# Performance work log

Measured on AMD Instinct MI355X. Metric: run time of the kernel, lower is better.

## Reference

```python
import jax, jax.numpy as jnp
import numpy as np

B, T, N, F_IN = 32, 64, 128, 16
H, SOUT = 64, 16
D = N * SOUT            # transformer d_model = 2048
NHEADS, DH = 16, 128
DFF, LAYERS = 2048, 2
NCLASSES, OUT = 8, 10
THR = 0.004             # edge threshold on sigmoid(V)/N


def setup_inputs():
    key = jax.random.key(0)
    ks = iter(jax.random.split(key, 40))
    r = lambda *s: jax.random.normal(next(ks), s, jnp.float32) * 0.02
    return {
        'X': jax.random.normal(next(ks), (B, T, N * F_IN), jnp.float32),
        'V_Adap': jax.random.normal(next(ks), (NCLASSES, N, N), jnp.float32),
        'Wl': r(F_IN, H), 'bl': jnp.zeros((H,)),
        'Wr': r(F_IN, H), 'br': jnp.zeros((H,)),
        'att': jax.random.normal(next(ks), (H,), jnp.float32) * 0.1,
        'gat_bias': jnp.zeros((H,)),
        'Wfc': r(H, SOUT), 'bfc': jnp.zeros((SOUT,)),
        'Wq': r(LAYERS, D, D), 'bq': jnp.zeros((LAYERS, D)),
        'Wk': r(LAYERS, D, D), 'bk': jnp.zeros((LAYERS, D)),
        'Wv': r(LAYERS, D, D), 'bv': jnp.zeros((LAYERS, D)),
        'Wo': r(LAYERS, D, D), 'bo': jnp.zeros((LAYERS, D)),
        'ln1_g': jnp.ones((LAYERS, D)), 'ln1_b': jnp.zeros((LAYERS, D)),
        'W1': r(LAYERS, D, DFF), 'b1': jnp.zeros((LAYERS, DFF)),
        'W2': r(LAYERS, DFF, D), 'b2': jnp.zeros((LAYERS, D)),
        'ln2_g': jnp.ones((LAYERS, D)), 'ln2_b': jnp.zeros((LAYERS, D)),
        'Wout': r(D, OUT), 'bout': jnp.zeros((OUT,)),
        'class_idx': 2,
    }


def _ln(x, g, b):
    mu = jnp.mean(x, -1, keepdims=True)
    var = jnp.var(x, -1, keepdims=True)
    return (x - mu) / jnp.sqrt(var + 1e-5) * g + b


def reference(X, V_Adap, Wl, bl, Wr, br, att, gat_bias, Wfc, bfc,
              Wq, bq, Wk, bk, Wv, bv, Wo, bo, ln1_g, ln1_b,
              W1, b1, W2, b2, ln2_g, ln2_b, Wout, bout, class_idx):
    # dynamic adjacency: sigmoid + scale + threshold (data-dependent sparsity as a mask)
    A = jax.nn.sigmoid(V_Adap[class_idx]) / N
    mask = (A > THR) | jnp.eye(N, dtype=bool)   # GATv2Conv default add_self_loops

    def gat_step(x_t):                           # x_t: (B, N, F_IN)
        xl = x_t @ Wl + bl                       # source transform (B, N, H)
        xr = x_t @ Wr + br                       # target transform (B, N, H)
        s = jax.nn.leaky_relu(xl[:, :, None, :] + xr[:, None, :, :], 0.2)  # (B, src, dst, H)
        e = jnp.where(mask[None], jnp.einsum('bijh,h->bij', s, att), -1e9)
        alpha = jax.nn.softmax(e, axis=1)        # softmax over sources per target node
        out = jnp.einsum('bij,bih->bjh', alpha, xl) + gat_bias
        return out @ Wfc + bfc                   # (B, N, SOUT)

    Xr = X.reshape(B, T, N, F_IN).transpose(1, 0, 2, 3)   # (T, B, N, F)
    spatial = jax.lax.map(gat_step, Xr)                   # (T, B, N, SOUT)
    h = spatial.transpose(1, 0, 2, 3).reshape(B, T, D)

    # post-norm TransformerEncoder (torch defaults: relu, d_ff=2048, no dropout at eval)
    for l in range(LAYERS):
        q = (h @ Wq[l] + bq[l]).reshape(B, T, NHEADS, DH).transpose(0, 2, 1, 3)
        k = (h @ Wk[l] + bk[l]).reshape(B, T, NHEADS, DH).transpose(0, 2, 1, 3)
        v = (h @ Wv[l] + bv[l]).reshape(B, T, NHEADS, DH).transpose(0, 2, 1, 3)
        aw = jax.nn.softmax(jnp.einsum('bhqd,bhkd->bhqk', q, k) / np.float32(np.sqrt(DH)), axis=-1)
        ao = jnp.einsum('bhqk,bhkd->bhqd', aw, v).transpose(0, 2, 1, 3).reshape(B, T, D)
        h = _ln(h + ao @ Wo[l] + bo[l], ln1_g[l], ln1_b[l])
        ff = jax.nn.relu(h @ W1[l] + b1[l]) @ W2[l] + b2[l]
        h = _ln(h + ff, ln2_g[l], ln2_b[l])

    return h[:, -1, :] @ Wout + bout             # (B, OUT)
```

## Files before the change

kernel.cpp:

```cpp
#include <hip/hip_runtime.h>
#include <cstdint>
#include <cstddef>


typedef unsigned short u16;
typedef __bf16 bf16x8 __attribute__((ext_vector_type(8)));
typedef float f32x4 __attribute__((ext_vector_type(4)));
typedef unsigned int u32x4 __attribute__((ext_vector_type(4)));
typedef float f32x4v __attribute__((ext_vector_type(4)));
typedef unsigned short u16x4 __attribute__((ext_vector_type(4)));

__device__ __forceinline__ u16 f2b(float f) {
  union { float f; unsigned u; } x; x.f = f;
  unsigned r = x.u + 0x7fffu + ((x.u >> 16) & 1u);
  return (u16)(r >> 16);
}
__device__ __forceinline__ float b2f(u16 s) {
  union { unsigned u; float f; } x; x.u = ((unsigned)s) << 16;
  return x.f;
}
__device__ __forceinline__ float b2f_lo(unsigned q) {
  union { unsigned u; float f; } x; x.u = q << 16;
  return x.f;
}
__device__ __forceinline__ float b2f_hi(unsigned q) {
  union { unsigned u; float f; } x; x.u = q & 0xffff0000u;
  return x.f;
}

__device__ __forceinline__ void gload_lds16(const void* g, void* l) {
  __builtin_amdgcn_global_load_lds(
      (const __attribute__((address_space(1))) unsigned int*)g,
      (__attribute__((address_space(3))) unsigned int*)l, 16, 0, 0);
}

__global__ __launch_bounds__(1024) void gat_kernel(
    const float* __restrict__ X, const float* __restrict__ V_Adap,
    const int* __restrict__ class_idx,
    const float* __restrict__ Wl, const float* __restrict__ bl,
    const float* __restrict__ Wr, const float* __restrict__ br,
    const float* __restrict__ att, const float* __restrict__ gat_bias,
    const float* __restrict__ Wfc, const float* __restrict__ bfc,
    float* __restrict__ h_f32, u16* __restrict__ h_b16)
{
  const int bt = blockIdx.x;
  const int tid = threadIdx.x;

  __shared__ __align__(16) float xlT[64 * 132];
  __shared__ __align__(16) float xrT[64 * 132];
  __shared__ __align__(16) u16   xlTb[64 * 136];
  __shared__ __align__(16) u16   esbT[128 * 136];
  __shared__ __align__(16) u16   aggb[128 * 72];
  __shared__ __align__(16) float WlT[64 * 20];
  __shared__ __align__(16) float WrT[64 * 20];
  __shared__ __align__(16) float WfcT[16 * 66];
  __shared__ float atts[64], bls[64], brs[64], gbias[64], bfcs[16];
  __shared__ float cls[128], crs[128], inv_s[128];
  __shared__ float red[8 * 128];

  {
    const int h = tid >> 4, f = tid & 15;
    WlT[h * 20 + f] = Wl[f * 64 + h];
    WrT[h * 20 + f] = Wr[f * 64 + h];
    WfcT[f * 66 + h] = Wfc[h * 16 + f];
  }
  if (tid < 64) { atts[tid] = att[tid]; bls[tid] = bl[tid]; brs[tid] = br[tid]; gbias[tid] = gat_bias[tid]; }
  if (tid < 16) bfcs[tid] = bfc[tid];
  const int cidx = *class_idx;
  __syncthreads();

  {
    const int n = tid >> 3, hq = tid & 7;
    const float* xp = X + (size_t)bt * 2048 + n * 16;
    float xv[16];
    #pragma unroll
    for (int f4 = 0; f4 < 4; f4++) {
      f32x4v t4 = ((const f32x4v*)xp)[f4];
      xv[f4 * 4 + 0] = t4[0]; xv[f4 * 4 + 1] = t4[1];
      xv[f4 * 4 + 2] = t4[2]; xv[f4 * 4 + 3] = t4[3];
    }
    #pragma unroll
    for (int k = 0; k < 8; k++) {
      const int h = hq + 8 * k;
      float al = bls[h], ar = brs[h];
      #pragma unroll
      for (int f4 = 0; f4 < 4; f4++) {
        f32x4v wl = *(const f32x4v*)&WlT[h * 20 + f4 * 4];
        f32x4v wr = *(const f32x4v*)&WrT[h * 20 + f4 * 4];
        #pragma unroll
        for (int f = 0; f < 4; f++) {
          al = fmaf(xv[f4 * 4 + f], wl[f], al);
          ar = fmaf(xv[f4 * 4 + f], wr[f], ar);
        }
      }
      xlT[h * 132 + n] = al;
      xrT[h * 132 + n] = ar;
      xlTb[h * 136 + n] = f2b(al);
    }
  }
  __syncthreads();

  if (tid < 256) {
    const int n = tid & 127;
    const float* srcT = (tid < 128) ? xlT : xrT;
    float s = 0.f;
    for (int h = 0; h < 64; h++) s = fmaf(atts[h], srcT[h * 132 + n], s);
    if (tid < 128) cls[n] = s; else crs[n] = s;
  }
  __syncthreads();

  {
    const int i0 = (tid >> 5) * 4;
    const int j0 = (tid & 31) * 4;
    float acc[4][4] = {};
    #pragma unroll 2
    for (int h = 0; h < 64; h++) {
      const float ah = atts[h];
      f32x4v xa = *(const f32x4v*)&xlT[h * 132 + i0];
      f32x4v xb = *(const f32x4v*)&xrT[h * 132 + j0];
      #pragma unroll
      for (int a = 0; a < 4; a++)
        #pragma unroll
        for (int b = 0; b < 4; b++)
          acc[a][b] = fmaf(ah, __builtin_fabsf(xa[a] + xb[b]), acc[a][b]);
    }
    const float* Vc = V_Adap + (size_t)cidx * 16384;
    float vm[4][4];
    #pragma unroll
    for (int a = 0; a < 4; a++) {
      f32x4v vc = *(const f32x4v*)&Vc[(size_t)(i0 + a) * 128 + j0];
      #pragma unroll
      for (int b = 0; b < 4; b++) vm[a][b] = vc[b];
    }
    #pragma unroll
    for (int b = 0; b < 4; b++) {
      const int j = j0 + b;
      const float ej = 0.6f * crs[j];
      u16x4 pk;
      #pragma unroll
      for (int a = 0; a < 4; a++) {
        const int i = i0 + a;
        const float e = ej + 0.6f * cls[i] + 0.4f * acc[a][b];
        const bool m = (vm[a][b] > 0.04800922f) || (i == j);
        pk[a] = f2b(m ? e : -1e9f);
      }
      *(u16x4*)&esbT[j * 136 + i0] = pk;
    }
  }
  __syncthreads();

  {
    const int j = tid >> 3, c = tid & 7;
    u16* rp = &esbT[j * 136 + c * 16];
    float ps = 0.f;
    #pragma unroll
    for (int half = 0; half < 2; half++) {
      u32x4 q = *(u32x4*)(rp + half * 8);
      #pragma unroll
      for (int w2 = 0; w2 < 4; w2++) {
        const float p0 = __expf(b2f_lo(q[w2]));
        const float p1 = __expf(b2f_hi(q[w2]));
        ps += p0 + p1;
        q[w2] = (unsigned)f2b(p0) | ((unsigned)f2b(p1) << 16);
      }
      *(u32x4*)(rp + half * 8) = q;
    }
    red[c * 128 + j] = ps;
  }
  __syncthreads();
  if (tid < 128) {
    float s = 0.f;
    #pragma unroll
    for (int c = 0; c < 8; c++) s += red[c * 128 + tid];
    inv_s[tid] = 1.f / s;
  }
  __syncthreads();

  {
    const int w = tid >> 6, lane = tid & 63;
    const int lq = lane >> 4, lr = lane & 15;
    const int jt = w >> 1, ht0 = (w & 1) * 2;
    f32x4 acc2[2] = {};
    #pragma unroll
    for (int ks = 0; ks < 4; ks++) {
      const bf16x8 af = __builtin_bit_cast(bf16x8,
          *(const u32x4*)&esbT[(jt * 16 + lr) * 136 + ks * 32 + lq * 8]);
      #pragma unroll
      for (int t = 0; t < 2; t++) {
        const bf16x8 bfb = __builtin_bit_cast(bf16x8,
            *(const u32x4*)&xlTb[((ht0 + t) * 16 + lr) * 136 + ks * 32 + lq * 8]);
        acc2[t] = __builtin_amdgcn_mfma_f32_16x16x32_bf16(af, bfb, acc2[t], 0, 0, 0);
      }
    }
    #pragma unroll
    for (int t = 0; t < 2; t++) {
      const int h = (ht0 + t) * 16 + lr;
      const float gb = gbias[h];
      #pragma unroll
      for (int r = 0; r < 4; r++) {
        const int j = jt * 16 + lq * 4 + r;
        aggb[j * 72 + h] = f2b(acc2[t][r] * inv_s[j] + gb);
      }
    }
  }
  __syncthreads();

  {
    const int j = tid >> 3, s0 = (tid & 7) * 2;
    float o0 = bfcs[s0], o1 = bfcs[s0 + 1];
    #pragma unroll
    for (int h8 = 0; h8 < 8; h8++) {
      u32x4 q = *(const u32x4*)&aggb[j * 72 + h8 * 8];
      #pragma unroll
      for (int w2 = 0; w2 < 4; w2++) {
        const int h = h8 * 8 + w2 * 2;
        const float a0 = b2f_lo(q[w2]);
        const float a1 = b2f_hi(q[w2]);
        o0 = fmaf(a0, WfcT[s0 * 66 + h], o0);
        o1 = fmaf(a0, WfcT[(s0 + 1) * 66 + h], o1);
        o0 = fmaf(a1, WfcT[s0 * 66 + h + 1], o0);
        o1 = fmaf(a1, WfcT[(s0 + 1) * 66 + h + 1], o1);
      }
    }
    const size_t off = (size_t)bt * 2048 + j * 16 + s0;
    h_f32[off] = o0; h_f32[off + 1] = o1;
    h_b16[off] = f2b(o0); h_b16[off + 1] = f2b(o1);
  }
}

struct TransArgs {
  const float* s0; const float* s1; const float* s2;
  u16* d0; u16* d1; u16* d2;
};

__global__ __launch_bounds__(256) void transpose_cast(TransArgs p)
{
  const float* src = (blockIdx.z == 0) ? p.s0 : (blockIdx.z == 1) ? p.s1 : p.s2;
  u16* dst = (blockIdx.z == 0) ? p.d0 : (blockIdx.z == 1) ? p.d1 : p.d2;
  __shared__ u16 tile[64][66];
  const int k0 = blockIdx.y * 64, n0 = blockIdx.x * 64;
  const int tid = threadIdx.x;
  const int c = tid & 63, rb = tid >> 6;
  #pragma unroll
  for (int r = 0; r < 16; r++) {
    const int k = rb + r * 4;
    tile[k][c] = f2b(src[(size_t)(k0 + k) * 2048 + n0 + c]);
  }
  __syncthreads();
  #pragma unroll
  for (int r = 0; r < 16; r++) {
    const int n = rb + r * 4;
    dst[(size_t)(n0 + n) * 2048 + k0 + c] = tile[c][n];
  }
}

struct GemmArgs {
  const u16* A;
  const u16* Bt0; const u16* Bt1; const u16* Bt2;
  const float* b0; const float* b1; const float* b2;
  void* C0; void* C1; void* C2;
  int N; int K;
};

template <int MODE>
__global__ __launch_bounds__(256) void gemm_bt(GemmArgs g)
{
  const int z = blockIdx.z;
  const u16* Bt = (z == 0) ? g.Bt0 : (z == 1) ? g.Bt1 : g.Bt2;
  const float* bias = (z == 0) ? g.b0 : (z == 1) ? g.b1 : g.b2;
  void* C = (z == 0) ? g.C0 : (z == 1) ? g.C1 : g.C2;
  const int N = g.N, K = g.K;
  const int m0 = blockIdx.y * 128, n0 = blockIdx.x * 128;

  __shared__ __align__(16) u16 As[2][128 * 32];
  __shared__ __align__(16) u16 Bs[2][128 * 32];

  const int tid = threadIdx.x;
  const int lane = tid & 63, w = tid >> 6;
  const int srow = w * 16 + (lane >> 2);
  const int scol = ((lane & 3) ^ ((lane >> 2) & 3)) * 8;
  const u16* gA = g.A + (size_t)(m0 + srow) * K + scol;
  const u16* gB = Bt + (size_t)(n0 + srow) * K + scol;
  const int lbase = (w * 16) * 32;

  const int wm = (w >> 1) * 64, wn = (w & 1) * 64;
  const int lq = lane >> 4, lr = lane & 15;
  const int csw = (lr & 3) << 3;

  f32x4 acc[4][4] = {};
  const int NT = K >> 5;

  auto stage = [&](int buf, int kt) {
    const int kk = kt << 5;
    #pragma unroll
    for (int c = 0; c < 2; c++) {
      gload_lds16(gA + (size_t)(c * 64) * K + kk, &As[buf][lbase + c * 64 * 32]);
      gload_lds16(gB + (size_t)(c * 64) * K + kk, &Bs[buf][lbase + c * 64 * 32]);
    }
  };
  auto compute = [&](int buf) {
    bf16x8 af[4], bfr[4];
    #pragma unroll
    for (int i = 0; i < 4; i++) {
      af[i] = __builtin_bit_cast(bf16x8,
          *(const u32x4*)&As[buf][(wm + i * 16 + lr) * 32 + ((lq * 8) ^ csw)]);
      bfr[i] = __builtin_bit_cast(bf16x8,
          *(const u32x4*)&Bs[buf][(wn + i * 16 + lr) * 32 + ((lq * 8) ^ csw)]);
    }
    #pragma unroll
    for (int mi = 0; mi < 4; mi++)
      #pragma unroll
      for (int ni = 0; ni < 4; ni++)
        acc[mi][ni] = __builtin_amdgcn_mfma_f32_16x16x32_bf16(af[mi], bfr[ni], acc[mi][ni], 0, 0, 0);
  };

  stage(0, 0);
  __syncthreads();
  int cur = 0;
  for (int kt = 0; kt + 1 < NT; ++kt) {
    stage(cur ^ 1, kt + 1);
    compute(cur);
    __syncthreads();
    cur ^= 1;
  }
  compute(cur);

  #pragma unroll
  for (int ni = 0; ni < 4; ni++) {
    const int col = n0 + wn + ni * 16 + lr;
    const float bv = bias[col];
    #pragma unroll
    for (int mi = 0; mi < 4; mi++) {
      #pragma unroll
      for (int r = 0; r < 4; r++) {
        const int row = m0 + wm + mi * 16 + lq * 4 + r;
        float v = acc[mi][ni][r] + bv;
        if (MODE == 0) {
          ((float*)C)[(size_t)row * N + col] = v;
        } else {
          if (MODE == 2) v = fmaxf(v, 0.f);
          ((u16*)C)[(size_t)row * N + col] = f2b(v);
        }
      }
    }
  }
}

template <int MODE>
__global__ __launch_bounds__(256) void gemm_bt64(GemmArgs g)
{
  const u16* Bt = g.Bt0;
  const float* bias = g.b0;
  void* C = g.C0;
  const int N = g.N, K = g.K;
  const int m0 = blockIdx.y * 128, n0 = blockIdx.x * 64;

  __shared__ __align__(16) u16 As[2][128 * 64];
  __shared__ __align__(16) u16 Bs[2][64 * 64];

  const int tid = threadIdx.x;
  const int lane = tid & 63, w = tid >> 6;
  const int srow = w * 8 + (lane >> 3);
  const int scol = ((lane & 7) ^ (lane >> 3)) * 8;
  const u16* gA = g.A + (size_t)(m0 + srow) * K + scol;
  const u16* gB = Bt + (size_t)(n0 + srow) * K + scol;
  const int lbase = (w * 8) * 64;

  const int wm = w * 32;
  const int lq = lane >> 4, lr = lane & 15;
  const int csw = (lr & 7) << 3;

  f32x4 acc[2][4] = {};
  const int NT = K >> 6;

  auto stage = [&](int buf, int kt) {
    const int kk = kt << 6;
    #pragma unroll
    for (int c = 0; c < 4; c++)
      gload_lds16(gA + (size_t)(c * 32) * K + kk, &As[buf][lbase + c * 32 * 64]);
    #pragma unroll
    for (int c = 0; c < 2; c++)
      gload_lds16(gB + (size_t)(c * 32) * K + kk, &Bs[buf][lbase + c * 32 * 64]);
  };
  auto compute = [&](int buf) {
    #pragma unroll
    for (int ks = 0; ks < 2; ks++) {
      bf16x8 af[2], bfr[4];
      #pragma unroll
      for (int i = 0; i < 2; i++)
        af[i] = __builtin_bit_cast(bf16x8,
            *(const u32x4*)&As[buf][(wm + i * 16 + lr) * 64 + ((ks * 32 + lq * 8) ^ csw)]);
      #pragma unroll
      for (int i = 0; i < 4; i++)
        bfr[i] = __builtin_bit_cast(bf16x8,
            *(const u32x4*)&Bs[buf][(i * 16 + lr) * 64 + ((ks * 32 + lq * 8) ^ csw)]);
      #pragma unroll
      for (int mi = 0; mi < 2; mi++)
        #pragma unroll
        for (int ni = 0; ni < 4; ni++)
          acc[mi][ni] = __builtin_amdgcn_mfma_f32_16x16x32_bf16(af[mi], bfr[ni], acc[mi][ni], 0, 0, 0);
    }
  };

  stage(0, 0);
  __syncthreads();
  int cur = 0;
  for (int kt = 0; kt + 1 < NT; ++kt) {
    stage(cur ^ 1, kt + 1);
    compute(cur);
    __syncthreads();
    cur ^= 1;
  }
  compute(cur);

  #pragma unroll
  for (int ni = 0; ni < 4; ni++) {
    const int col = n0 + ni * 16 + lr;
    const float bv = bias[col];
    #pragma unroll
    for (int mi = 0; mi < 2; mi++) {
      #pragma unroll
      for (int r = 0; r < 4; r++) {
        const int row = m0 + wm + mi * 16 + lq * 4 + r;
        float v = acc[mi][ni][r] + bv;
        if (MODE == 0) {
          ((float*)C)[(size_t)row * N + col] = v;
        } else {
          if (MODE == 2) v = fmaxf(v, 0.f);
          ((u16*)C)[(size_t)row * N + col] = f2b(v);
        }
      }
    }
  }
}

__global__ __launch_bounds__(256) void attn_kernel(
    const u16* __restrict__ Qb, const u16* __restrict__ Kb,
    const u16* __restrict__ Vb, u16* __restrict__ AOb)
{
  const int head = blockIdx.x, b = blockIdx.y;
  const int tid = threadIdx.x;
  __shared__ __align__(16) float qs[64 * 132];
  __shared__ __align__(16) float ks[64 * 132];
  __shared__ __align__(16) float vs[64 * 128];
  __shared__ __align__(16) float ss[64 * 65];
  const size_t base = ((size_t)b * 64) * 2048 + (size_t)head * 128;

  for (int idx = tid; idx < 1024; idx += 256) {
    const int t_ = idx >> 4, d8 = (idx & 15) * 8;
    const size_t gp = base + (size_t)t_ * 2048 + d8;
    const u32x4 q = *(const u32x4*)(Qb + gp);
    const u32x4 k = *(const u32x4*)(Kb + gp);
    const u32x4 v = *(const u32x4*)(Vb + gp);
    f32x4 q0 = {b2f_lo(q[0]), b2f_hi(q[0]), b2f_lo(q[1]), b2f_hi(q[1])};
    f32x4 q1 = {b2f_lo(q[2]), b2f_hi(q[2]), b2f_lo(q[3]), b2f_hi(q[3])};
    f32x4 k0 = {b2f_lo(k[0]), b2f_hi(k[0]), b2f_lo(k[1]), b2f_hi(k[1])};
    f32x4 k1 = {b2f_lo(k[2]), b2f_hi(k[2]), b2f_lo(k[3]), b2f_hi(k[3])};
    f32x4 v0 = {b2f_lo(v[0]), b2f_hi(v[0]), b2f_lo(v[1]), b2f_hi(v[1])};
    f32x4 v1 = {b2f_lo(v[2]), b2f_hi(v[2]), b2f_lo(v[3]), b2f_hi(v[3])};
    *(f32x4*)&qs[t_ * 132 + d8] = q0; *(f32x4*)&qs[t_ * 132 + d8 + 4] = q1;
    *(f32x4*)&ks[t_ * 132 + d8] = k0; *(f32x4*)&ks[t_ * 132 + d8 + 4] = k1;
    *(f32x4*)&vs[t_ * 128 + d8] = v0; *(f32x4*)&vs[t_ * 128 + d8 + 4] = v1;
  }
  __syncthreads();

  {
    const int i0 = (tid >> 4) * 4, j0 = tid & 15;
    float acc[4][4] = {};
    #pragma unroll 2
    for (int d0 = 0; d0 < 128; d0 += 4) {
      f32x4 qv[4], kv[4];
      #pragma unroll
      for (int a = 0; a < 4; a++) qv[a] = *(const f32x4*)&qs[(i0 + a) * 132 + d0];
      #pragma unroll
      for (int c = 0; c < 4; c++) kv[c] = *(const f32x4*)&ks[(j0 + c * 16) * 132 + d0];
      #pragma unroll
      for (int a = 0; a < 4; a++)
        #pragma unroll
        for (int c = 0; c < 4; c++)
          #pragma unroll
          for (int e = 0; e < 4; e++)
            acc[a][c] = fmaf(qv[a][e], kv[c][e], acc[a][c]);
    }
    const float sc = 0.08838834764831845f;
    #pragma unroll
    for (int a = 0; a < 4; a++)
      #pragma unroll
      for (int c = 0; c < 4; c++)
        ss[(i0 + a) * 65 + j0 + c * 16] = acc[a][c] * sc;
  }
  __syncthreads();

  {
    const int row = tid >> 2;
    float* rp = &ss[row * 65 + (tid & 3) * 16];
    float mx = -3e38f;
    #pragma unroll
    for (int j = 0; j < 16; j++) mx = fmaxf(mx, rp[j]);
    mx = fmaxf(mx, __shfl_xor(mx, 1, 64));
    mx = fmaxf(mx, __shfl_xor(mx, 2, 64));
    float s = 0.f;
    #pragma unroll
    for (int j = 0; j < 16; j++) { const float p = __expf(rp[j] - mx); rp[j] = p; s += p; }
    s += __shfl_xor(s, 1, 64);
    s += __shfl_xor(s, 2, 64);
    const float inv = 1.f / s;
    #pragma unroll
    for (int j = 0; j < 16; j++) rp[j] *= inv;
  }
  __syncthreads();

  {
    const int i0 = (tid >> 4) * 4, d0 = (tid & 15) * 8;
    float o[4][8] = {};
    for (int j = 0; j < 64; j++) {
      float pv[4];
      #pragma unroll
      for (int a = 0; a < 4; a++) pv[a] = ss[(i0 + a) * 65 + j];
      f32x4v v0 = *(const f32x4v*)&vs[j * 128 + d0];
      f32x4v v1 = *(const f32x4v*)&vs[j * 128 + d0 + 4];
      float vv[8] = {v0[0], v0[1], v0[2], v0[3], v1[0], v1[1], v1[2], v1[3]};
      #pragma unroll
      for (int a = 0; a < 4; a++)
        #pragma unroll
        for (int c = 0; c < 8; c++)
          o[a][c] = fmaf(pv[a], vv[c], o[a][c]);
    }
    #pragma unroll
    for (int a = 0; a < 4; a++)
      #pragma unroll
      for (int c = 0; c < 8; c++)
        AOb[base + (size_t)(i0 + a) * 2048 + d0 + c] = f2b(o[a][c]);
  }
}

__global__ __launch_bounds__(256) void ln_kernel(
    const float* __restrict__ hin, const float* __restrict__ delta,
    const float* __restrict__ gamma, const float* __restrict__ beta,
    float* __restrict__ hout, u16* __restrict__ bout_)
{
  const int token = blockIdx.x, tid = threadIdx.x;
  const size_t off = (size_t)token * 2048;
  __shared__ float red[8];
  f32x4 v[2];
  float s = 0.f;
  #pragma unroll
  for (int r = 0; r < 2; r++) {
    const int i = r * 1024 + tid * 4;
    const f32x4 a = *(const f32x4*)(hin + off + i);
    const f32x4 b = *(const f32x4*)(delta + off + i);
    v[r] = a + b;
    s += v[r][0] + v[r][1] + v[r][2] + v[r][3];
  }
  #pragma unroll
  for (int o = 32; o > 0; o >>= 1) s += __shfl_down(s, o, 64);
  if ((tid & 63) == 0) red[tid >> 6] = s;
  __syncthreads();
  const float mean = (red[0] + red[1] + red[2] + red[3]) * (1.f / 2048.f);
  float s2 = 0.f;
  #pragma unroll
  for (int r = 0; r < 2; r++)
    #pragma unroll
    for (int e = 0; e < 4; e++) { const float d = v[r][e] - mean; s2 = fmaf(d, d, s2); }
  #pragma unroll
  for (int o = 32; o > 0; o >>= 1) s2 += __shfl_down(s2, o, 64);
  if ((tid & 63) == 0) red[4 + (tid >> 6)] = s2;
  __syncthreads();
  const float var = (red[4] + red[5] + red[6] + red[7]) * (1.f / 2048.f);
  const float rstd = rsqrtf(var + 1e-5f);
  #pragma unroll
  for (int r = 0; r < 2; r++) {
    const int i = r * 1024 + tid * 4;
    const f32x4 gm = *(const f32x4*)(gamma + i);
    const f32x4 bt = *(const f32x4*)(beta + i);
    f32x4 y;
    u16x4 pb;
    #pragma unroll
    for (int e = 0; e < 4; e++) {
      y[e] = (v[r][e] - mean) * rstd * gm[e] + bt[e];
      pb[e] = f2b(y[e]);
    }
    *(f32x4*)(hout + off + i) = y;
    *(u16x4*)(bout_ + off + i) = pb;
  }
}

__global__ __launch_bounds__(256) void final_kernel(
    const float* __restrict__ h, const float* __restrict__ Wout,
    const float* __restrict__ bout, float* __restrict__ out)
{
  const int b = blockIdx.x, tid = threadIdx.x;
  __shared__ float row[2048];
  __shared__ float part[256];
  const float* hr = h + ((size_t)b * 64 + 63) * 2048;
  for (int i = tid; i < 2048; i += 256) row[i] = hr[i];
  __syncthreads();
  const int o = tid & 15, ch = tid >> 4;
  float s = 0.f;
  if (o < 10) {
    const int i0 = ch * 128;
    for (int i = i0; i < i0 + 128; i++) s = fmaf(row[i], Wout[(size_t)i * 10 + o], s);
  }
  part[tid] = s;
  __syncthreads();
  if (tid < 10) {
    float t = bout[tid];
    for (int c2 = 0; c2 < 16; c2++) t += part[c2 * 16 + tid];
    out[(size_t)b * 10 + tid] = t;
  }
}

extern "C" void kernel_launch(void* const* d_in, const int* in_sizes, int n_in,
                              void* d_out, int out_size, void* d_ws, size_t ws_size,
                              hipStream_t stream)
{
  const float* X        = (const float*)d_in[0];
  const float* V_Adap   = (const float*)d_in[1];
  const float* Wl       = (const float*)d_in[2];
  const float* bl       = (const float*)d_in[3];
  const float* Wr       = (const float*)d_in[4];
  const float* br       = (const float*)d_in[5];
  const float* att      = (const float*)d_in[6];
  const float* gat_bias = (const float*)d_in[7];
  const float* Wfc      = (const float*)d_in[8];
  const float* bfc      = (const float*)d_in[9];
  const float* Wq       = (const float*)d_in[10];
  const float* bq       = (const float*)d_in[11];
  const float* Wk       = (const float*)d_in[12];
  const float* bk       = (const float*)d_in[13];
  const float* Wv       = (const float*)d_in[14];
  const float* bv       = (const float*)d_in[15];
  const float* Wo       = (const float*)d_in[16];
  const float* bo       = (const float*)d_in[17];
  const float* ln1_g    = (const float*)d_in[18];
  const float* ln1_b    = (const float*)d_in[19];
  const float* W1       = (const float*)d_in[20];
  const float* b1       = (const float*)d_in[21];
  const float* W2       = (const float*)d_in[22];
  const float* b2       = (const float*)d_in[23];
  const float* ln2_g    = (const float*)d_in[24];
  const float* ln2_b    = (const float*)d_in[25];
  const float* WoutP    = (const float*)d_in[26];
  const float* boutP    = (const float*)d_in[27];
  const int*   class_idx = (const int*)d_in[28];

  char* ws = (char*)d_ws;
  const size_t MB = (size_t)1 << 20;
  float* h_f32 = (float*)(ws);
  u16*   h_b16 = (u16*)(ws + 16 * MB);
  u16*   Qb    = (u16*)(ws + 24 * MB);
  u16*   Kb    = (u16*)(ws + 32 * MB);
  u16*   Vb    = (u16*)(ws + 40 * MB);
  u16*   AOb   = (u16*)(ws + 48 * MB);
  float* tmp   = (float*)(ws + 56 * MB);
  u16*   ff1b  = (u16*)(ws + 72 * MB);
  u16*   Wt0   = (u16*)(ws + 80 * MB);
  u16*   Wt1   = (u16*)(ws + 88 * MB);
  u16*   Wt2   = (u16*)(ws + 96 * MB);

  gat_kernel<<<2048, 1024, 0, stream>>>(X, V_Adap, class_idx, Wl, bl, Wr, br,
                                        att, gat_bias, Wfc, bfc, h_f32, h_b16);

  const size_t DD = 2048ull * 2048ull;
  for (int l = 0; l < 2; l++) {
    const size_t wofs = (size_t)l * DD;
    const size_t bofs = (size_t)l * 2048;

    transpose_cast<<<dim3(32, 32, 3), 256, 0, stream>>>(
        TransArgs{Wq + wofs, Wk + wofs, Wv + wofs, Wt0, Wt1, Wt2});
    gemm_bt<1><<<dim3(16, 16, 3), 256, 0, stream>>>(
        GemmArgs{h_b16, Wt0, Wt1, Wt2, bq + bofs, bk + bofs, bv + bofs,
                 Qb, Kb, Vb, 2048, 2048});

    attn_kernel<<<dim3(16, 32), 256, 0, stream>>>(Qb, Kb, Vb, AOb);

    transpose_cast<<<dim3(32, 32, 3), 256, 0, stream>>>(
        TransArgs{Wo + wofs, W1 + wofs, W2 + wofs, Wt0, Wt1, Wt2});

    gemm_bt64<0><<<dim3(32, 16), 256, 0, stream>>>(
        GemmArgs{AOb, Wt0, nullptr, nullptr, bo + bofs, nullptr, nullptr,
                 tmp, nullptr, nullptr, 2048, 2048});
    ln_kernel<<<2048, 256, 0, stream>>>(h_f32, tmp, ln1_g + bofs, ln1_b + bofs,
                                        h_f32, h_b16);

    gemm_bt64<2><<<dim3(32, 16), 256, 0, stream>>>(
        GemmArgs{h_b16, Wt1, nullptr, nullptr, b1 + bofs, nullptr, nullptr,
                 ff1b, nullptr, nullptr, 2048, 2048});

    gemm_bt64<0><<<dim3(32, 16), 256, 0, stream>>>(
        GemmArgs{ff1b, Wt2, nullptr, nullptr, b2 + bofs, nullptr, nullptr,
                 tmp, nullptr, nullptr, 2048, 2048});
    ln_kernel<<<2048, 256, 0, stream>>>(h_f32, tmp, ln2_g + bofs, ln2_b + bofs,
                                        h_f32, h_b16);
  }

  final_kernel<<<32, 256, 0, stream>>>(h_f32, WoutP, boutP, (float*)d_out);
}
```

Baseline: 907.0 us.

## Restructure GAT projection, attention-coefficient reduction and edge-score tiling

```diff
diff --git a/kernel.cpp b/kernel.cpp
--- a/kernel.cpp
+++ b/kernel.cpp
@@ -6,6 +6,7 @@
 typedef unsigned short u16;
 typedef __bf16 bf16x8 __attribute__((ext_vector_type(8)));
 typedef float f32x4 __attribute__((ext_vector_type(4)));
+typedef float f32x2 __attribute__((ext_vector_type(2)));
 typedef unsigned int u32x4 __attribute__((ext_vector_type(4)));
 typedef float f32x4v __attribute__((ext_vector_type(4)));
 typedef unsigned short u16x4 __attribute__((ext_vector_type(4)));
@@ -58,6 +59,8 @@
   __shared__ float cls[128], crs[128], inv_s[128];
   __shared__ float red[8 * 128];
 
+  float* scratchX = (float*)aggb;
+
   {
     const int h = tid >> 4, f = tid & 15;
     WlT[h * 20 + f] = Wl[f * 64 + h];
@@ -66,85 +69,110 @@
   }
   if (tid < 64) { atts[tid] = att[tid]; bls[tid] = bl[tid]; brs[tid] = br[tid]; gbias[tid] = gat_bias[tid]; }
   if (tid < 16) bfcs[tid] = bfc[tid];
+  if (tid < 512)
+    ((f32x4*)scratchX)[tid] = ((const f32x4*)(X + (size_t)bt * 2048))[tid];
   const int cidx = *class_idx;
   __syncthreads();
 
   {
-    const int n = tid >> 3, hq = tid & 7;
-    const float* xp = X + (size_t)bt * 2048 + n * 16;
-    float xv[16];
+    const int h = tid & 63, ng = tid >> 6;
+    f32x4 wl4[4], wr4[4];
     #pragma unroll
     for (int f4 = 0; f4 < 4; f4++) {
-      f32x4v t4 = ((const f32x4v*)xp)[f4];
-      xv[f4 * 4 + 0] = t4[0]; xv[f4 * 4 + 1] = t4[1];
-      xv[f4 * 4 + 2] = t4[2]; xv[f4 * 4 + 3] = t4[3];
-    }
-    #pragma unroll
-    for (int k = 0; k < 8; k++) {
-      const int h = hq + 8 * k;
-      float al = bls[h], ar = brs[h];
+      wl4[f4] = *(const f32x4*)&WlT[h * 20 + f4 * 4];
+      wr4[f4] = *(const f32x4*)&WrT[h * 20 + f4 * 4];
+    }
+    const float blh = bls[h], brh = brs[h];
+    float al8[8], ar8[8];
+    #pragma unroll
+    for (int t = 0; t < 8; t++) {
+      const int n = ng * 8 + t;
+      float al = blh, ar = brh;
       #pragma unroll
       for (int f4 = 0; f4 < 4; f4++) {
-        f32x4v wl = *(const f32x4v*)&WlT[h * 20 + f4 * 4];
-        f32x4v wr = *(const f32x4v*)&WrT[h * 20 + f4 * 4];
+        const f32x4 xv = *(const f32x4*)&scratchX[n * 16 + f4 * 4];
         #pragma unroll
         for (int f = 0; f < 4; f++) {
-          al = fmaf(xv[f4 * 4 + f], wl[f], al);
-          ar = fmaf(xv[f4 * 4 + f], wr[f], ar);
+          al = fmaf(xv[f], wl4[f4][f], al);
+          ar = fmaf(xv[f], wr4[f4][f], ar);
         }
       }
-      xlT[h * 132 + n] = al;
-      xrT[h * 132 + n] = ar;
-      xlTb[h * 136 + n] = f2b(al);
-    }
-  }
-  __syncthreads();
-
+      al8[t] = al; ar8[t] = ar;
+    }
+    *(f32x4*)&xlT[h * 132 + ng * 8]     = *(f32x4*)&al8[0];
+    *(f32x4*)&xlT[h * 132 + ng * 8 + 4] = *(f32x4*)&al8[4];
+    *(f32x4*)&xrT[h * 132 + ng * 8]     = *(f32x4*)&ar8[0];
+    *(f32x4*)&xrT[h * 132 + ng * 8 + 4] = *(f32x4*)&ar8[4];
+    u16 pb[8];
+    #pragma unroll
+    for (int t = 0; t < 8; t++) pb[t] = f2b(al8[t]);
+    *(u16x4*)&xlTb[h * 136 + ng * 8]     = *(u16x4*)&pb[0];
+    *(u16x4*)&xlTb[h * 136 + ng * 8 + 4] = *(u16x4*)&pb[4];
+  }
+  __syncthreads();
+
+  {
+    const int n = tid & 127, g = tid >> 7;
+    const float* srcT = (g < 4) ? xlT : xrT;
+    const int h0 = (g & 3) * 16;
+    float s = 0.f;
+    #pragma unroll
+    for (int hh = 0; hh < 16; hh++)
+      s = fmaf(atts[h0 + hh], srcT[(h0 + hh) * 132 + n], s);
+    red[g * 128 + n] = s;
+  }
+  __syncthreads();
   if (tid < 256) {
     const int n = tid & 127;
-    const float* srcT = (tid < 128) ? xlT : xrT;
-    float s = 0.f;
-    for (int h = 0; h < 64; h++) s = fmaf(atts[h], srcT[h * 132 + n], s);
+    const int base = (tid < 128) ? 0 : 4;
+    const float s = ((red[base * 128 + n] + red[(base + 1) * 128 + n])
+                   + red[(base + 2) * 128 + n]) + red[(base + 3) * 128 + n];
     if (tid < 128) cls[n] = s; else crs[n] = s;
   }
   __syncthreads();
 
   {
-    const int i0 = (tid >> 5) * 4;
-    const int j0 = (tid & 31) * 4;
-    float acc[4][4] = {};
-    #pragma unroll 2
+    const int i0 = (tid >> 6) * 8;
+    const int j0 = (tid & 63) * 2;
+    float acc[8][2] = {};
+    #pragma unroll 8
     for (int h = 0; h < 64; h++) {
-      const float ah = atts[h];
-      f32x4v xa = *(const f32x4v*)&xlT[h * 132 + i0];
-      f32x4v xb = *(const f32x4v*)&xrT[h * 132 + j0];
-      #pragma unroll
-      for (int a = 0; a < 4; a++)
-        #pragma unroll
-        for (int b = 0; b < 4; b++)
-          acc[a][b] = fmaf(ah, __builtin_fabsf(xa[a] + xb[b]), acc[a][b]);
+      const float ah = att[h];
+      const f32x4 xa0 = *(const f32x4*)&xlT[h * 132 + i0];
+      const f32x4 xa1 = *(const f32x4*)&xlT[h * 132 + i0 + 4];
+      const f32x2 xb  = *(const f32x2*)&xrT[h * 132 + j0];
+      #pragma unroll
+      for (int a = 0; a < 4; a++) {
+        acc[a][0]     = fmaf(ah, __builtin_fabsf(xa0[a] + xb[0]), acc[a][0]);
+        acc[a][1]     = fmaf(ah, __builtin_fabsf(xa0[a] + xb[1]), acc[a][1]);
+        acc[4 + a][0] = fmaf(ah, __builtin_fabsf(xa1[a] + xb[0]), acc[4 + a][0]);
+        acc[4 + a][1] = fmaf(ah, __builtin_fabsf(xa1[a] + xb[1]), acc[4 + a][1]);
+      }
     }
     const float* Vc = V_Adap + (size_t)cidx * 16384;
-    float vm[4][4];
-    #pragma unroll
-    for (int a = 0; a < 4; a++) {
-      f32x4v vc = *(const f32x4v*)&Vc[(size_t)(i0 + a) * 128 + j0];
-      #pragma unroll
-      for (int b = 0; b < 4; b++) vm[a][b] = vc[b];
-    }
-    #pragma unroll
-    for (int b = 0; b < 4; b++) {
+    float vm[8][2];
+    #pragma unroll
+    for (int a = 0; a < 8; a++) {
+      const f32x2 vc = *(const f32x2*)&Vc[(size_t)(i0 + a) * 128 + j0];
+      vm[a][0] = vc[0]; vm[a][1] = vc[1];
+    }
+    const f32x4 cl0 = *(const f32x4*)&cls[i0];
+    const f32x4 cl1 = *(const f32x4*)&cls[i0 + 4];
+    float cli[8] = {cl0[0], cl0[1], cl0[2], cl0[3], cl1[0], cl1[1], cl1[2], cl1[3]};
+    #pragma unroll
+    for (int b = 0; b < 2; b++) {
       const int j = j0 + b;
       const float ej = 0.6f * crs[j];
-      u16x4 pk;
-      #pragma unroll
-      for (int a = 0; a < 4; a++) {
+      u16 pk[8];
+      #pragma unroll
+      for (int a = 0; a < 8; a++) {
         const int i = i0 + a;
-        const float e = ej + 0.6f * cls[i] + 0.4f * acc[a][b];
+        const float e = ej + 0.6f * cli[a] + 0.4f * acc[a][b];
         const bool m = (vm[a][b] > 0.04800922f) || (i == j);
         pk[a] = f2b(m ? e : -1e9f);
       }
-      *(u16x4*)&esbT[j * 136 + i0] = pk;
+      *(u16x4*)&esbT[j * 136 + i0]     = *(u16x4*)&pk[0];
+      *(u16x4*)&esbT[j * 136 + i0 + 4] = *(u16x4*)&pk[4];
     }
   }
   __syncthreads();
```

Result: no change. 891.0 us (-1.8%).
